# Kernel tuning notes

Measured on AMD Instinct MI355X. Metric: run time of the kernel, lower is better.

## Reference

```python
import jax, jax.numpy as jnp
import numpy as np

NUM_EXPERTS = 8
GROUP_SIZE = 2
NUM_GROUPS = NUM_EXPERTS // GROUP_SIZE
NUM_SLOTS = 128
HIDDEN = 2048
D_FF = int(HIDDEN * 4 * (2.0 / 3.0))  # 5461
BATCH = 4
SEQ = 2048
BS = BATCH * SEQ


def setup_inputs() -> dict:
    key = jax.random.key(0)
    k0, k1, k2, k3 = jax.random.split(key, 4)
    x = jax.random.normal(k0, (BS, HIDDEN), dtype=jnp.float32)
    router_weights = jax.random.normal(k1, (BS, NUM_EXPERTS), dtype=jnp.float32)
    up_w = jax.random.normal(k2, (NUM_GROUPS, HIDDEN, D_FF), dtype=jnp.float32) * np.float32(1.0 / np.sqrt(HIDDEN))
    up_b = jnp.zeros((NUM_GROUPS, D_FF), dtype=jnp.float32)
    down_w = jax.random.normal(k3, (NUM_EXPERTS, D_FF, HIDDEN), dtype=jnp.float32) * np.float32(1.0 / np.sqrt(D_FF))
    down_b = jnp.zeros((NUM_EXPERTS, HIDDEN), dtype=jnp.float32)
    return {
        "x": x,
        "router_weights": router_weights,
        "up_w": up_w,
        "up_b": up_b,
        "down_w": down_w,
        "down_b": down_b,
        "batch_size": BATCH,
        "seq_len": SEQ,
    }


def reference(x, router_weights, up_w, up_b, down_w, down_b, batch_size, seq_len):
    # --- soft routing matrices (Soft-MoE; source raises NotImplementedError) ---
    h = router_weights                                   # (bs, E) routing logits
    dispatch = jax.nn.softmax(h, axis=0)                 # normalize over tokens per expert
    P = jnp.broadcast_to(dispatch[:, None, :], (h.shape[0], NUM_SLOTS, NUM_EXPERTS))  # (bs, k, E)
    G = jnp.full((NUM_SLOTS, NUM_EXPERTS), 1.0 / NUM_SLOTS, dtype=x.dtype)            # expert-choice combine (k, E)

    # --- dispatch: expert slot inputs ---
    tokens_for_expert = jnp.einsum('bke,bh->ekh', P, x)  # (E, k, hidden)

    # --- per-expert FFN (grouped up proj shared within each expert group) ---
    group_idx = np.arange(NUM_EXPERTS) // GROUP_SIZE     # static gather of shared up weights
    up_w_e = up_w[group_idx]                             # (E, hidden, d_ff)
    up_b_e = up_b[group_idx]                             # (E, d_ff)
    mid = jax.nn.silu(jnp.einsum('ekh,ehf->ekf', tokens_for_expert, up_w_e) + up_b_e[:, None, :])
    E_out = jnp.einsum('ekf,efh->ekh', mid, down_w) + down_b[:, None, :]  # (E, k, hidden)

    # --- combine (expert-choice branch): 'bs k e, k e, e k h -> bs h' ---
    y = jnp.einsum('bke,ke,ekh->bh', P, G, E_out)
    return y.reshape(batch_size, seq_len, HIDDEN)
```

## Files before the change

### kernel.cpp

```cpp
#include <hip/hip_runtime.h>

typedef float f4 __attribute__((ext_vector_type(4)));

#define HID 2048
#define DFF 5461
#define NE  8

#define WS_IS 0
#define WS_T  64
#define WS_EO 16448

#define SC_TP 0
#define SC_TS 1048576
#define SC_MP 1049600
#define SC_EP 1748736

__global__ __launch_bounds__(256) void k_tpart(const float* __restrict__ x,
                                               const float* __restrict__ rw,
                                               float* __restrict__ sc) {
  __shared__ f4 dv4[64][2];
  __shared__ f4 red[3][NE][64];
  int tid = threadIdx.x;
  int rc = blockIdx.y;
  int col = tid & 63, rg = tid >> 6;
  int c4 = blockIdx.x * 64 + col;
  const f4* x4 = (const f4*)x;
  f4 acc[NE];
#pragma unroll
  for (int e = 0; e < NE; e++) acc[e] = (f4){0.f, 0.f, 0.f, 0.f};
  double spart = 0.0;
  for (int sub = 0; sub < 2; sub++) {
    int b0 = rc * 128 + sub * 64;
    if (tid < 128) {
      int row = tid >> 1, half = tid & 1;
      const float* rp = rw + (size_t)(b0 + row) * NE + half * 4;
      f4 d;
      d.x = __expf(rp[0]);
      d.y = __expf(rp[1]);
      d.z = __expf(rp[2]);
      d.w = __expf(rp[3]);
      dv4[row][half] = d;
    }
    __syncthreads();
    if (blockIdx.x == 0 && tid < NE) {
      const float* dp = (const float*)dv4;
      for (int row = 0; row < 64; row++) spart += (double)dp[row * 8 + tid];
    }
#pragma unroll 4
    for (int r = 0; r < 16; r++) {
      int row = rg * 16 + r;
      f4 xv = __builtin_nontemporal_load(&x4[(size_t)(b0 + row) * 512 + c4]);
      f4 dlo = dv4[row][0], dhi = dv4[row][1];
      acc[0] += dlo.x * xv;
      acc[1] += dlo.y * xv;
      acc[2] += dlo.z * xv;
      acc[3] += dlo.w * xv;
      acc[4] += dhi.x * xv;
      acc[5] += dhi.y * xv;
      acc[6] += dhi.z * xv;
      acc[7] += dhi.w * xv;
    }
    __syncthreads();
  }
  if (blockIdx.x == 0 && tid < NE) sc[SC_TS + rc * NE + tid] = (float)spart;
  if (rg) {
#pragma unroll
    for (int e = 0; e < NE; e++) red[rg - 1][e][col] = acc[e];
  }
  __syncthreads();
  if (!rg) {
    f4* o4 = (f4*)(sc + SC_TP);
#pragma unroll
    for (int e = 0; e < NE; e++) {
      f4 a = acc[e] + red[0][e][col] + red[1][e][col] + red[2][e][col];
      o4[(size_t)(rc * NE + e) * 512 + c4] = a;
    }
  }
}

__global__ __launch_bounds__(256) void k_tred(const float* __restrict__ sc,
                                              float* __restrict__ ws) {
  __shared__ float red[8][32];
  __shared__ float sinv[NE];
  int tid = threadIdx.x;
  if (tid < NE) {
    double s = 0.0;
    for (int ch = 0; ch < 64; ch++) s += (double)sc[SC_TS + ch * NE + tid];
    float inv = (float)(1.0 / s);
    sinv[tid] = inv;
    if (blockIdx.x == 0) ws[WS_IS + tid] = inv;
  }
  int o = tid & 31, grp = tid >> 5;
  int i = blockIdx.x * 32 + o;
  double a = 0.0;
#pragma unroll 4
  for (int k = 0; k < 8; k++)
    a += (double)sc[SC_TP + (size_t)(grp * 8 + k) * (NE * HID) + i];
  red[grp][o] = (float)a;
  __syncthreads();
  if (tid < 32) {
    int ii = blockIdx.x * 32 + tid;
    float s = 0.f;
#pragma unroll
    for (int g = 0; g < 8; g++) s += red[g][tid];
    ws[WS_T + ii] = s * sinv[ii >> 11];
  }
}

__global__ __launch_bounds__(256) void k_midpart(const float* __restrict__ up_w,
                                                 const float* __restrict__ ws,
                                                 float* __restrict__ sc) {
  int fb = blockIdx.x, hc = blockIdx.y, g = blockIdx.z;
  int tid = threadIdx.x;
  __shared__ float t0[128], t1[128];
  int h0 = hc * 128;
  if (tid < 128) t0[tid] = ws[WS_T + (2 * g) * HID + h0 + tid];
  else t1[tid - 128] = ws[WS_T + (2 * g + 1) * HID + h0 + tid - 128];
  __syncthreads();
  int fA = fb * 512 + tid;
  int fB = fA + 256;
  bool hasB = fB < DFF;
  const float* wp = up_w + ((size_t)g * HID + h0) * DFF;
  float a0 = 0.f, a1 = 0.f, bb0 = 0.f, bb1 = 0.f;
#pragma unroll 8
  for (int h = 0; h < 128; h++) {
    float wA = __builtin_nontemporal_load(wp + (size_t)h * DFF + fA);
    float wB = hasB ? __builtin_nontemporal_load(wp + (size_t)h * DFF + fB) : 0.f;
    a0 += t0[h] * wA;
    a1 += t1[h] * wA;
    bb0 += t0[h] * wB;
    bb1 += t1[h] * wB;
  }
  float* mp = sc + SC_MP + (size_t)hc * NE * DFF;
  mp[(size_t)(2 * g) * DFF + fA] = a0;
  mp[(size_t)(2 * g + 1) * DFF + fA] = a1;
  if (hasB) {
    mp[(size_t)(2 * g) * DFF + fB] = bb0;
    mp[(size_t)(2 * g + 1) * DFF + fB] = bb1;
  }
}

__global__ __launch_bounds__(256) void k_eopart(const float* __restrict__ down_w,
                                                const float* __restrict__ up_b,
                                                const float* __restrict__ sc_mp,
                                                float* __restrict__ sc) {
  int hb = blockIdx.x, fc = blockIdx.y, e = blockIdx.z;
  int tid = threadIdx.x;
  int f0 = fc * 43;
  const f4* base4 = (const f4*)down_w + ((size_t)e * DFF + f0) * 512 + hb * 256 + tid;
  f4 w[8];
#pragma unroll
  for (int j = 0; j < 8; j++)
    w[j] = __builtin_nontemporal_load(&base4[(size_t)j * 512]);
  __shared__ float ml[4][43];
  int lane = tid & 63, wv = tid >> 6;
  if (lane < 43) {
    double a = (double)up_b[(size_t)(e >> 1) * DFF + f0 + lane];
#pragma unroll 4
    for (int k = 0; k < 16; k++)
      a += (double)sc_mp[SC_MP + (size_t)(k * NE + e) * DFF + f0 + lane];
    float af = (float)a;
    ml[wv][lane] = af / (1.f + __expf(-af));
  }
  f4 acc = (f4){0.f, 0.f, 0.f, 0.f};
  for (int blk = 0; blk < 5; blk++) {
#pragma unroll
    for (int j = 0; j < 8; j++) {
      int cur = blk * 8 + j;
      f4 c = w[j];
      int nxt = cur + 8;
      if (nxt < 43) w[j] = __builtin_nontemporal_load(&base4[(size_t)nxt * 512]);
      acc += ml[wv][cur] * c;
    }
  }
#pragma unroll
  for (int j = 0; j < 3; j++) acc += ml[wv][40 + j] * w[j];
  ((f4*)(sc + SC_EP))[(size_t)(fc * NE + e) * 512 + hb * 256 + tid] = acc;
}

__global__ __launch_bounds__(256) void k_eored(const float* __restrict__ sc,
                                               const float* __restrict__ down_b,
                                               float* __restrict__ ws) {
  __shared__ float red[8][32];
  int tid = threadIdx.x;
  int o = tid & 31, grp = tid >> 5;
  int i = blockIdx.x * 32 + o;
  double a = 0.0;
  for (int fc = grp; fc < 127; fc += 8)
    a += (double)sc[SC_EP + (size_t)fc * (NE * HID) + i];
  red[grp][o] = (float)a;
  __syncthreads();
  if (tid < 32) {
    int ii = blockIdx.x * 32 + tid;
    float s = down_b[ii];
#pragma unroll
    for (int g = 0; g < 8; g++) s += red[g][tid];
    ws[WS_EO + ii] = s;
  }
}

__global__ __launch_bounds__(256) void k_comb(const float* __restrict__ rw,
                                              const float* __restrict__ ws,
                                              float* __restrict__ y) {
  int tid = threadIdx.x;
  int b0 = blockIdx.x * 16;
  __shared__ float dvl[16][NE];
  if (tid < 128) {
    int tok = tid >> 3, e = tid & 7;
    dvl[tok][e] = __expf(rw[(size_t)(b0 + tok) * NE + e]) * ws[WS_IS + e];
  }
  __syncthreads();
  const f4* eo4 = (const f4*)(ws + WS_EO);
  f4 ea[NE], eb[NE];
#pragma unroll
  for (int e = 0; e < NE; e++) {
    ea[e] = eo4[e * 512 + tid];
    eb[e] = eo4[e * 512 + 256 + tid];
  }
  f4* y4 = (f4*)y;
#pragma unroll 4
  for (int t = 0; t < 16; t++) {
    f4 o0 = (f4){0.f, 0.f, 0.f, 0.f};
    f4 o1 = (f4){0.f, 0.f, 0.f, 0.f};
#pragma unroll
    for (int e = 0; e < NE; e++) {
      float d = dvl[t][e];
      o0 += d * ea[e];
      o1 += d * eb[e];
    }
    __builtin_nontemporal_store(o0, &y4[(size_t)(b0 + t) * 512 + tid]);
    __builtin_nontemporal_store(o1, &y4[(size_t)(b0 + t) * 512 + 256 + tid]);
  }
}

extern "C" void kernel_launch(void* const* d_in, const int* in_sizes, int n_in,
                              void* d_out, int out_size, void* d_ws, size_t ws_size,
                              hipStream_t stream) {
  const float* x      = (const float*)d_in[0];
  const float* rw     = (const float*)d_in[1];
  const float* up_w   = (const float*)d_in[2];
  const float* up_b   = (const float*)d_in[3];
  const float* down_w = (const float*)d_in[4];
  const float* down_b = (const float*)d_in[5];
  float* y  = (float*)d_out;
  float* ws = (float*)d_ws;
  float* sc = y;

  hipLaunchKernelGGL(k_tpart, dim3(8, 64), dim3(256), 0, stream, x, rw, sc);
  hipLaunchKernelGGL(k_tred, dim3(512), dim3(256), 0, stream, sc, ws);
  hipLaunchKernelGGL(k_midpart, dim3(11, 16, 4), dim3(256), 0, stream, up_w, ws, sc);
  hipLaunchKernelGGL(k_eopart, dim3(2, 127, 8), dim3(256), 0, stream, down_w, up_b, sc, sc);
  hipLaunchKernelGGL(k_eored, dim3(512), dim3(256), 0, stream, sc, down_b, ws);
  hipLaunchKernelGGL(k_comb, dim3(512), dim3(256), 0, stream, rw, ws, y);
}
```

Baseline: 132.1 us.

## Fold token-reduction kernel into up-projection and rebalance split-K grids

Removes the separate k_tred launch. Each k_midpart block now reduces the 64 per-chunk partial token sums for its own slice and computes the softmax normalizers itself, and k_comb recomputes the inverse sums. k_midpart's grid changes to 16 f-blocks of 342 with bounds checks, and k_eopart's f-chunk doubles to 86, which halves the partials k_eored has to reduce. The cost is redundant reduction work: every midpart block re-reads 64 partial rows for its slice, repeated across all f-blocks.

```diff
diff --git a/kernel.cpp b/kernel.cpp
--- a/kernel.cpp
+++ b/kernel.cpp
@@ -6,18 +6,17 @@
 #define DFF 5461
 #define NE  8
 
-#define WS_IS 0
-#define WS_T  64
-#define WS_EO 16448
+#define WS_TS 0
+#define WS_EO 1024
 
 #define SC_TP 0
-#define SC_TS 1048576
-#define SC_MP 1049600
-#define SC_EP 1748736
+#define SC_MP 1048576
+#define SC_EP 1747584
 
 __global__ __launch_bounds__(256) void k_tpart(const float* __restrict__ x,
                                                const float* __restrict__ rw,
-                                               float* __restrict__ sc) {
+                                               float* __restrict__ sc,
+                                               float* __restrict__ wsb) {
   __shared__ f4 dv4[64][2];
   __shared__ f4 red[3][NE][64];
   int tid = threadIdx.x;
@@ -46,7 +45,7 @@
       const float* dp = (const float*)dv4;
       for (int row = 0; row < 64; row++) spart += (double)dp[row * 8 + tid];
     }
-#pragma unroll 4
+#pragma unroll 8
     for (int r = 0; r < 16; r++) {
       int row = rg * 16 + r;
       f4 xv = __builtin_nontemporal_load(&x4[(size_t)(b0 + row) * 512 + c4]);
@@ -62,7 +61,7 @@
     }
     __syncthreads();
   }
-  if (blockIdx.x == 0 && tid < NE) sc[SC_TS + rc * NE + tid] = (float)spart;
+  if (blockIdx.x == 0 && tid < NE) wsb[WS_TS + rc * NE + tid] = (float)spart;
   if (rg) {
 #pragma unroll
     for (int e = 0; e < NE; e++) red[rg - 1][e][col] = acc[e];
@@ -78,53 +77,43 @@
   }
 }
 
-__global__ __launch_bounds__(256) void k_tred(const float* __restrict__ sc,
-                                              float* __restrict__ ws) {
-  __shared__ float red[8][32];
-  __shared__ float sinv[NE];
-  int tid = threadIdx.x;
-  if (tid < NE) {
-    double s = 0.0;
-    for (int ch = 0; ch < 64; ch++) s += (double)sc[SC_TS + ch * NE + tid];
-    float inv = (float)(1.0 / s);
-    sinv[tid] = inv;
-    if (blockIdx.x == 0) ws[WS_IS + tid] = inv;
-  }
-  int o = tid & 31, grp = tid >> 5;
-  int i = blockIdx.x * 32 + o;
-  double a = 0.0;
-#pragma unroll 4
-  for (int k = 0; k < 8; k++)
-    a += (double)sc[SC_TP + (size_t)(grp * 8 + k) * (NE * HID) + i];
-  red[grp][o] = (float)a;
-  __syncthreads();
-  if (tid < 32) {
-    int ii = blockIdx.x * 32 + tid;
-    float s = 0.f;
-#pragma unroll
-    for (int g = 0; g < 8; g++) s += red[g][tid];
-    ws[WS_T + ii] = s * sinv[ii >> 11];
-  }
-}
-
 __global__ __launch_bounds__(256) void k_midpart(const float* __restrict__ up_w,
-                                                 const float* __restrict__ ws,
+                                                 const float* __restrict__ sc_tp,
+                                                 const float* __restrict__ wsb,
                                                  float* __restrict__ sc) {
   int fb = blockIdx.x, hc = blockIdx.y, g = blockIdx.z;
   int tid = threadIdx.x;
   __shared__ float t0[128], t1[128];
+  __shared__ float s01[2];
   int h0 = hc * 128;
-  if (tid < 128) t0[tid] = ws[WS_T + (2 * g) * HID + h0 + tid];
-  else t1[tid - 128] = ws[WS_T + (2 * g + 1) * HID + h0 + tid - 128];
-  __syncthreads();
-  int fA = fb * 512 + tid;
+  if (tid < 2) {
+    double s = 0.0;
+    for (int ch = 0; ch < 64; ch++)
+      s += (double)wsb[WS_TS + ch * NE + 2 * g + tid];
+    s01[tid] = (float)(1.0 / s);
+  }
+  {
+    int half = tid >> 7, h = tid & 127;
+    double a = 0.0;
+    for (int ch = 0; ch < 64; ch++)
+      a += (double)sc_tp[SC_TP + (size_t)(ch * NE + 2 * g + half) * HID + h0 + h];
+    if (half == 0) t0[h] = (float)a;
+    else t1[h] = (float)a;
+  }
+  __syncthreads();
+  if (tid < 128) t0[tid] *= s01[0];
+  else t1[tid - 128] *= s01[1];
+  __syncthreads();
+  int fstart = fb * 342;
+  int fend = min(fstart + 342, DFF);
+  int fA = fstart + tid;
   int fB = fA + 256;
-  bool hasB = fB < DFF;
+  bool hasA = fA < fend, hasB = fB < fend;
   const float* wp = up_w + ((size_t)g * HID + h0) * DFF;
   float a0 = 0.f, a1 = 0.f, bb0 = 0.f, bb1 = 0.f;
 #pragma unroll 8
   for (int h = 0; h < 128; h++) {
-    float wA = __builtin_nontemporal_load(wp + (size_t)h * DFF + fA);
+    float wA = hasA ? __builtin_nontemporal_load(wp + (size_t)h * DFF + fA) : 0.f;
     float wB = hasB ? __builtin_nontemporal_load(wp + (size_t)h * DFF + fB) : 0.f;
     a0 += t0[h] * wA;
     a1 += t1[h] * wA;
@@ -132,8 +121,10 @@
     bb1 += t1[h] * wB;
   }
   float* mp = sc + SC_MP + (size_t)hc * NE * DFF;
-  mp[(size_t)(2 * g) * DFF + fA] = a0;
-  mp[(size_t)(2 * g + 1) * DFF + fA] = a1;
+  if (hasA) {
+    mp[(size_t)(2 * g) * DFF + fA] = a0;
+    mp[(size_t)(2 * g + 1) * DFF + fA] = a1;
+  }
   if (hasB) {
     mp[(size_t)(2 * g) * DFF + fB] = bb0;
     mp[(size_t)(2 * g + 1) * DFF + fB] = bb1;
@@ -146,47 +137,51 @@
                                                 float* __restrict__ sc) {
   int hb = blockIdx.x, fc = blockIdx.y, e = blockIdx.z;
   int tid = threadIdx.x;
-  int f0 = fc * 43;
+  int f0 = fc * 86;
+  int nf = min(86, DFF - f0);
   const f4* base4 = (const f4*)down_w + ((size_t)e * DFF + f0) * 512 + hb * 256 + tid;
   f4 w[8];
 #pragma unroll
   for (int j = 0; j < 8; j++)
     w[j] = __builtin_nontemporal_load(&base4[(size_t)j * 512]);
-  __shared__ float ml[4][43];
+  __shared__ float ml[4][86];
   int lane = tid & 63, wv = tid >> 6;
-  if (lane < 43) {
-    double a = (double)up_b[(size_t)(e >> 1) * DFF + f0 + lane];
+  for (int f = lane; f < nf; f += 64) {
+    double a = (double)up_b[(size_t)(e >> 1) * DFF + f0 + f];
 #pragma unroll 4
     for (int k = 0; k < 16; k++)
-      a += (double)sc_mp[SC_MP + (size_t)(k * NE + e) * DFF + f0 + lane];
+      a += (double)sc_mp[SC_MP + (size_t)(k * NE + e) * DFF + f0 + f];
     float af = (float)a;
-    ml[wv][lane] = af / (1.f + __expf(-af));
+    ml[wv][f] = af / (1.f + __expf(-af));
   }
   f4 acc = (f4){0.f, 0.f, 0.f, 0.f};
-  for (int blk = 0; blk < 5; blk++) {
+  int nfull = nf >> 3;
+  int ntail = nf & 7;
+  for (int blk = 0; blk < nfull; blk++) {
 #pragma unroll
     for (int j = 0; j < 8; j++) {
       int cur = blk * 8 + j;
       f4 c = w[j];
       int nxt = cur + 8;
-      if (nxt < 43) w[j] = __builtin_nontemporal_load(&base4[(size_t)nxt * 512]);
+      if (nxt < nf) w[j] = __builtin_nontemporal_load(&base4[(size_t)nxt * 512]);
       acc += ml[wv][cur] * c;
     }
   }
 #pragma unroll
-  for (int j = 0; j < 3; j++) acc += ml[wv][40 + j] * w[j];
+  for (int j = 0; j < 8; j++)
+    if (j < ntail) acc += ml[wv][nfull * 8 + j] * w[j];
   ((f4*)(sc + SC_EP))[(size_t)(fc * NE + e) * 512 + hb * 256 + tid] = acc;
 }
 
 __global__ __launch_bounds__(256) void k_eored(const float* __restrict__ sc,
                                                const float* __restrict__ down_b,
-                                               float* __restrict__ ws) {
+                                               float* __restrict__ wsb) {
   __shared__ float red[8][32];
   int tid = threadIdx.x;
   int o = tid & 31, grp = tid >> 5;
   int i = blockIdx.x * 32 + o;
   double a = 0.0;
-  for (int fc = grp; fc < 127; fc += 8)
+  for (int fc = grp; fc < 64; fc += 8)
     a += (double)sc[SC_EP + (size_t)fc * (NE * HID) + i];
   red[grp][o] = (float)a;
   __syncthreads();
@@ -195,28 +190,35 @@
     float s = down_b[ii];
 #pragma unroll
     for (int g = 0; g < 8; g++) s += red[g][tid];
-    ws[WS_EO + ii] = s;
+    wsb[WS_EO + ii] = s;
   }
 }
 
 __global__ __launch_bounds__(256) void k_comb(const float* __restrict__ rw,
-                                              const float* __restrict__ ws,
+                                              const float* __restrict__ wsb,
                                               float* __restrict__ y) {
   int tid = threadIdx.x;
   int b0 = blockIdx.x * 16;
   __shared__ float dvl[16][NE];
-  if (tid < 128) {
-    int tok = tid >> 3, e = tid & 7;
-    dvl[tok][e] = __expf(rw[(size_t)(b0 + tok) * NE + e]) * ws[WS_IS + e];
-  }
-  __syncthreads();
-  const f4* eo4 = (const f4*)(ws + WS_EO);
+  __shared__ float sinv[NE];
+  const f4* eo4 = (const f4*)(wsb + WS_EO);
   f4 ea[NE], eb[NE];
 #pragma unroll
   for (int e = 0; e < NE; e++) {
     ea[e] = eo4[e * 512 + tid];
     eb[e] = eo4[e * 512 + 256 + tid];
   }
+  if (tid < NE) {
+    double s = 0.0;
+    for (int ch = 0; ch < 64; ch++) s += (double)wsb[WS_TS + ch * NE + tid];
+    sinv[tid] = (float)(1.0 / s);
+  }
+  __syncthreads();
+  if (tid < 128) {
+    int tok = tid >> 3, e = tid & 7;
+    dvl[tok][e] = __expf(rw[(size_t)(b0 + tok) * NE + e]) * sinv[e];
+  }
+  __syncthreads();
   f4* y4 = (f4*)y;
 #pragma unroll 4
   for (int t = 0; t < 16; t++) {
@@ -242,14 +244,13 @@
   const float* up_b   = (const float*)d_in[3];
   const float* down_w = (const float*)d_in[4];
   const float* down_b = (const float*)d_in[5];
-  float* y  = (float*)d_out;
-  float* ws = (float*)d_ws;
-  float* sc = y;
-
-  hipLaunchKernelGGL(k_tpart, dim3(8, 64), dim3(256), 0, stream, x, rw, sc);
-  hipLaunchKernelGGL(k_tred, dim3(512), dim3(256), 0, stream, sc, ws);
-  hipLaunchKernelGGL(k_midpart, dim3(11, 16, 4), dim3(256), 0, stream, up_w, ws, sc);
-  hipLaunchKernelGGL(k_eopart, dim3(2, 127, 8), dim3(256), 0, stream, down_w, up_b, sc, sc);
-  hipLaunchKernelGGL(k_eored, dim3(512), dim3(256), 0, stream, sc, down_b, ws);
-  hipLaunchKernelGGL(k_comb, dim3(512), dim3(256), 0, stream, rw, ws, y);
-}
+  float* y   = (float*)d_out;
+  float* wsb = (float*)d_ws;
+  float* sc  = y;
+
+  hipLaunchKernelGGL(k_tpart, dim3(8, 64), dim3(256), 0, stream, x, rw, sc, wsb);
+  hipLaunchKernelGGL(k_midpart, dim3(16, 16, 4), dim3(256), 0, stream, up_w, sc, wsb, sc);
+  hipLaunchKernelGGL(k_eopart, dim3(2, 64, 8), dim3(256), 0, stream, down_w, up_b, sc, sc);
+  hipLaunchKernelGGL(k_eored, dim3(512), dim3(256), 0, stream, sc, down_b, wsb);
+  hipLaunchKernelGGL(k_comb, dim3(512), dim3(256), 0, stream, rw, wsb, y);
+}
```

Result: slower. 190.1 us (+43.9%).

## Fuse all MoE stages into one persistent cooperative kernel with grid syncs

Applied to the files above, without the earlier changes.

Combines the six separate stage kernels into a single cooperative kernel. Each stage becomes a grid-stride loop over its original virtual blocks, separated by grid.sync(), and the stages share one union of shared memory. The aim is to remove per-launch overhead and the idle gaps between dependent kernels. In exchange it adds grid-wide barrier costs and caps the grid at occupancy-limited resident blocks, which may hurt load balance in the larger stages. The x-read loop unroll also goes from 4 to 8, and the old multi-kernel path is kept as a fallback if the cooperative launch fails.

```diff
diff --git a/kernel.cpp b/kernel.cpp
--- a/kernel.cpp
+++ b/kernel.cpp
@@ -1,4 +1,7 @@
 #include <hip/hip_runtime.h>
+#include <hip/hip_cooperative_groups.h>
+
+namespace cg = cooperative_groups;
 
 typedef float f4 __attribute__((ext_vector_type(4)));
 
@@ -14,6 +17,231 @@
 #define SC_TS 1048576
 #define SC_MP 1049600
 #define SC_EP 1748736
+
+union SMem {
+  struct { f4 dv4[64][2]; f4 red[3][NE][64]; } tp;
+  struct { float red[8][32]; float sinv[NE]; } tr;
+  struct { float t0[128]; float t1[128]; } mp;
+  struct { float ml[4][43]; } eo;
+  struct { float red[8][32]; } er;
+  struct { float dvl[16][NE]; } cb;
+};
+
+__global__ __launch_bounds__(256) void k_fused(
+    const float* __restrict__ x, const float* __restrict__ rw,
+    const float* __restrict__ up_w, const float* __restrict__ up_b,
+    const float* __restrict__ down_w, const float* __restrict__ down_b,
+    float* __restrict__ y, float* __restrict__ ws) {
+  cg::grid_group grid = cg::this_grid();
+  __shared__ SMem sm;
+  int tid = threadIdx.x;
+  float* sc = y;
+  const int nb = gridDim.x;
+
+  for (int vb = blockIdx.x; vb < 512; vb += nb) {
+    int bxc = vb & 7, rc = vb >> 3;
+    int col = tid & 63, rg = tid >> 6;
+    int c4 = bxc * 64 + col;
+    const f4* x4 = (const f4*)x;
+    f4 acc[NE];
+#pragma unroll
+    for (int e = 0; e < NE; e++) acc[e] = (f4){0.f, 0.f, 0.f, 0.f};
+    double spart = 0.0;
+    for (int sub = 0; sub < 2; sub++) {
+      int b0 = rc * 128 + sub * 64;
+      if (tid < 128) {
+        int row = tid >> 1, half = tid & 1;
+        const float* rp = rw + (size_t)(b0 + row) * NE + half * 4;
+        f4 d;
+        d.x = __expf(rp[0]);
+        d.y = __expf(rp[1]);
+        d.z = __expf(rp[2]);
+        d.w = __expf(rp[3]);
+        sm.tp.dv4[row][half] = d;
+      }
+      __syncthreads();
+      if (bxc == 0 && tid < NE) {
+        const float* dp = (const float*)sm.tp.dv4;
+        for (int row = 0; row < 64; row++) spart += (double)dp[row * 8 + tid];
+      }
+#pragma unroll 8
+      for (int r = 0; r < 16; r++) {
+        int row = rg * 16 + r;
+        f4 xv = __builtin_nontemporal_load(&x4[(size_t)(b0 + row) * 512 + c4]);
+        f4 dlo = sm.tp.dv4[row][0], dhi = sm.tp.dv4[row][1];
+        acc[0] += dlo.x * xv;
+        acc[1] += dlo.y * xv;
+        acc[2] += dlo.z * xv;
+        acc[3] += dlo.w * xv;
+        acc[4] += dhi.x * xv;
+        acc[5] += dhi.y * xv;
+        acc[6] += dhi.z * xv;
+        acc[7] += dhi.w * xv;
+      }
+      __syncthreads();
+    }
+    if (bxc == 0 && tid < NE) sc[SC_TS + rc * NE + tid] = (float)spart;
+    if (rg) {
+#pragma unroll
+      for (int e = 0; e < NE; e++) sm.tp.red[rg - 1][e][col] = acc[e];
+    }
+    __syncthreads();
+    if (!rg) {
+      f4* o4 = (f4*)(sc + SC_TP);
+#pragma unroll
+      for (int e = 0; e < NE; e++) {
+        f4 a = acc[e] + sm.tp.red[0][e][col] + sm.tp.red[1][e][col] +
+               sm.tp.red[2][e][col];
+        o4[(size_t)(rc * NE + e) * 512 + c4] = a;
+      }
+    }
+    __syncthreads();
+  }
+  grid.sync();
+
+  for (int vb = blockIdx.x; vb < 512; vb += nb) {
+    if (tid < NE) {
+      double s = 0.0;
+      for (int ch = 0; ch < 64; ch++) s += (double)sc[SC_TS + ch * NE + tid];
+      float inv = (float)(1.0 / s);
+      sm.tr.sinv[tid] = inv;
+      if (vb == 0) ws[WS_IS + tid] = inv;
+    }
+    int o = tid & 31, grp = tid >> 5;
+    int i = vb * 32 + o;
+    double a = 0.0;
+#pragma unroll 4
+    for (int k = 0; k < 8; k++)
+      a += (double)sc[SC_TP + (size_t)(grp * 8 + k) * (NE * HID) + i];
+    sm.tr.red[grp][o] = (float)a;
+    __syncthreads();
+    if (tid < 32) {
+      int ii = vb * 32 + tid;
+      float s = 0.f;
+#pragma unroll
+      for (int g = 0; g < 8; g++) s += sm.tr.red[g][tid];
+      ws[WS_T + ii] = s * sm.tr.sinv[ii >> 11];
+    }
+    __syncthreads();
+  }
+  grid.sync();
+
+  for (int vb = blockIdx.x; vb < 704; vb += nb) {
+    int fb = vb % 11, hc = (vb / 11) & 15, g = vb / 176;
+    int h0 = hc * 128;
+    if (tid < 128) sm.mp.t0[tid] = ws[WS_T + (2 * g) * HID + h0 + tid];
+    else sm.mp.t1[tid - 128] = ws[WS_T + (2 * g + 1) * HID + h0 + tid - 128];
+    __syncthreads();
+    int fA = fb * 512 + tid;
+    int fB = fA + 256;
+    bool hasB = fB < DFF;
+    const float* wp = up_w + ((size_t)g * HID + h0) * DFF;
+    float a0 = 0.f, a1 = 0.f, bb0 = 0.f, bb1 = 0.f;
+#pragma unroll 8
+    for (int h = 0; h < 128; h++) {
+      float wA = __builtin_nontemporal_load(wp + (size_t)h * DFF + fA);
+      float wB = hasB ? __builtin_nontemporal_load(wp + (size_t)h * DFF + fB) : 0.f;
+      a0 += sm.mp.t0[h] * wA;
+      a1 += sm.mp.t1[h] * wA;
+      bb0 += sm.mp.t0[h] * wB;
+      bb1 += sm.mp.t1[h] * wB;
+    }
+    float* mp = sc + SC_MP + (size_t)hc * NE * DFF;
+    mp[(size_t)(2 * g) * DFF + fA] = a0;
+    mp[(size_t)(2 * g + 1) * DFF + fA] = a1;
+    if (hasB) {
+      mp[(size_t)(2 * g) * DFF + fB] = bb0;
+      mp[(size_t)(2 * g + 1) * DFF + fB] = bb1;
+    }
+    __syncthreads();
+  }
+  grid.sync();
+
+  for (int vb = blockIdx.x; vb < 2032; vb += nb) {
+    int hb = vb & 1, fc = (vb >> 1) % 127, e = vb / 254;
+    int f0 = fc * 43;
+    const f4* base4 =
+        (const f4*)down_w + ((size_t)e * DFF + f0) * 512 + hb * 256 + tid;
+    f4 w[8];
+#pragma unroll
+    for (int j = 0; j < 8; j++)
+      w[j] = __builtin_nontemporal_load(&base4[(size_t)j * 512]);
+    int lane = tid & 63, wv = tid >> 6;
+    if (lane < 43) {
+      double a = (double)up_b[(size_t)(e >> 1) * DFF + f0 + lane];
+#pragma unroll 4
+      for (int k = 0; k < 16; k++)
+        a += (double)sc[SC_MP + (size_t)(k * NE + e) * DFF + f0 + lane];
+      float af = (float)a;
+      sm.eo.ml[wv][lane] = af / (1.f + __expf(-af));
+    }
+    f4 acc = (f4){0.f, 0.f, 0.f, 0.f};
+    for (int blk = 0; blk < 5; blk++) {
+#pragma unroll
+      for (int j = 0; j < 8; j++) {
+        int cur = blk * 8 + j;
+        f4 c = w[j];
+        int nxt = cur + 8;
+        if (nxt < 43) w[j] = __builtin_nontemporal_load(&base4[(size_t)nxt * 512]);
+        acc += sm.eo.ml[wv][cur] * c;
+      }
+    }
+#pragma unroll
+    for (int j = 0; j < 3; j++) acc += sm.eo.ml[wv][40 + j] * w[j];
+    ((f4*)(sc + SC_EP))[(size_t)(fc * NE + e) * 512 + hb * 256 + tid] = acc;
+  }
+  grid.sync();
+
+  for (int vb = blockIdx.x; vb < 512; vb += nb) {
+    int o = tid & 31, grp = tid >> 5;
+    int i = vb * 32 + o;
+    double a = 0.0;
+    for (int fc = grp; fc < 127; fc += 8)
+      a += (double)sc[SC_EP + (size_t)fc * (NE * HID) + i];
+    sm.er.red[grp][o] = (float)a;
+    __syncthreads();
+    if (tid < 32) {
+      int ii = vb * 32 + tid;
+      float s = down_b[ii];
+#pragma unroll
+      for (int g = 0; g < 8; g++) s += sm.er.red[g][tid];
+      ws[WS_EO + ii] = s;
+    }
+    __syncthreads();
+  }
+  grid.sync();
+
+  for (int vb = blockIdx.x; vb < 512; vb += nb) {
+    int b0 = vb * 16;
+    if (tid < 128) {
+      int tok = tid >> 3, e = tid & 7;
+      sm.cb.dvl[tok][e] = __expf(rw[(size_t)(b0 + tok) * NE + e]) * ws[WS_IS + e];
+    }
+    __syncthreads();
+    const f4* eo4 = (const f4*)(ws + WS_EO);
+    f4 ea[NE], eb[NE];
+#pragma unroll
+    for (int e = 0; e < NE; e++) {
+      ea[e] = eo4[e * 512 + tid];
+      eb[e] = eo4[e * 512 + 256 + tid];
+    }
+    f4* y4 = (f4*)y;
+#pragma unroll 4
+    for (int t = 0; t < 16; t++) {
+      f4 o0 = (f4){0.f, 0.f, 0.f, 0.f};
+      f4 o1 = (f4){0.f, 0.f, 0.f, 0.f};
+#pragma unroll
+      for (int e = 0; e < NE; e++) {
+        float d = sm.cb.dvl[t][e];
+        o0 += d * ea[e];
+        o1 += d * eb[e];
+      }
+      __builtin_nontemporal_store(o0, &y4[(size_t)(b0 + t) * 512 + tid]);
+      __builtin_nontemporal_store(o1, &y4[(size_t)(b0 + t) * 512 + 256 + tid]);
+    }
+    __syncthreads();
+  }
+}
 
 __global__ __launch_bounds__(256) void k_tpart(const float* __restrict__ x,
                                                const float* __restrict__ rw,
@@ -46,7 +274,7 @@
       const float* dp = (const float*)dv4;
       for (int row = 0; row < 64; row++) spart += (double)dp[row * 8 + tid];
     }
-#pragma unroll 4
+#pragma unroll 8
     for (int r = 0; r < 16; r++) {
       int row = rg * 16 + r;
       f4 xv = __builtin_nontemporal_load(&x4[(size_t)(b0 + row) * 512 + c4]);
@@ -246,10 +474,25 @@
   float* ws = (float*)d_ws;
   float* sc = y;
 
-  hipLaunchKernelGGL(k_tpart, dim3(8, 64), dim3(256), 0, stream, x, rw, sc);
-  hipLaunchKernelGGL(k_tred, dim3(512), dim3(256), 0, stream, sc, ws);
-  hipLaunchKernelGGL(k_midpart, dim3(11, 16, 4), dim3(256), 0, stream, up_w, ws, sc);
-  hipLaunchKernelGGL(k_eopart, dim3(2, 127, 8), dim3(256), 0, stream, down_w, up_b, sc, sc);
-  hipLaunchKernelGGL(k_eored, dim3(512), dim3(256), 0, stream, sc, down_b, ws);
-  hipLaunchKernelGGL(k_comb, dim3(512), dim3(256), 0, stream, rw, ws, y);
-}
+  int maxB = 0;
+  hipError_t qerr =
+      hipOccupancyMaxActiveBlocksPerMultiprocessor(&maxB, k_fused, 256, 0);
+  int grid = (qerr == hipSuccess && maxB > 0) ? maxB * 256 : 0;
+  if (grid > 2032) grid = 2032;
+
+  hipError_t lerr = hipErrorUnknown;
+  if (grid > 0) {
+    void* args[] = {(void*)&x, (void*)&rw, (void*)&up_w, (void*)&up_b,
+                    (void*)&down_w, (void*)&down_b, (void*)&y, (void*)&ws};
+    lerr = hipLaunchCooperativeKernel((const void*)k_fused, dim3(grid),
+                                      dim3(256), args, 0, stream);
+  }
+  if (lerr != hipSuccess) {
+    hipLaunchKernelGGL(k_tpart, dim3(8, 64), dim3(256), 0, stream, x, rw, sc);
+    hipLaunchKernelGGL(k_tred, dim3(512), dim3(256), 0, stream, sc, ws);
+    hipLaunchKernelGGL(k_midpart, dim3(11, 16, 4), dim3(256), 0, stream, up_w, ws, sc);
+    hipLaunchKernelGGL(k_eopart, dim3(2, 127, 8), dim3(256), 0, stream, down_w, up_b, sc, sc);
+    hipLaunchKernelGGL(k_eored, dim3(512), dim3(256), 0, stream, sc, down_b, ws);
+    hipLaunchKernelGGL(k_comb, dim3(512), dim3(256), 0, stream, rw, ws, y);
+  }
+}
```

Measured after the change: 316.1 us. 2.39x slower.
